# Optimization experiments

Measured on AMD Instinct MI355X. Metric: run time of the kernel, lower is better.

## Reference

```python
import jax, jax.numpy as jnp
import numpy as np

F_DIM = 256
N_HEADS = 4
D_Q = F_DIM // N_HEADS  # 64
EPS = 1e-6


def layer_norm(x, g, b):
    mu = jnp.mean(x, axis=-1, keepdims=True)
    var = jnp.mean(jnp.square(x - mu), axis=-1, keepdims=True)
    return (x - mu) * jax.lax.rsqrt(var + EPS) * g + b


def linear(x, W, b):
    # torch nn.Linear: y = x @ W.T + b, W: [out, in]
    return jnp.einsum('...i,oi->...o', x, W) + b


def setup_inputs() -> dict:
    key = jax.random.key(0)
    ks = jax.random.split(key, 16)
    f = F_DIM
    inp = {
        'code_map': jax.random.normal(ks[0], (8, 512, f), jnp.float32),
        'texture_map': jax.random.normal(ks[1], (8, 512, f), jnp.float32),
        'Wq': jax.random.normal(ks[2], (N_HEADS * D_Q, f), jnp.float32) * 0.02,
        'bq': jnp.zeros((N_HEADS * D_Q,), jnp.float32),
        'Wk': jax.random.normal(ks[3], (N_HEADS * D_Q, f), jnp.float32) * 0.02,
        'bk': jnp.zeros((N_HEADS * D_Q,), jnp.float32),
        'Wv': jax.random.normal(ks[4], (N_HEADS * D_Q, f), jnp.float32) * 0.02,
        'bv': jnp.zeros((N_HEADS * D_Q,), jnp.float32),
        'Wo': jax.random.normal(ks[5], (f, N_HEADS * D_Q), jnp.float32) * 0.02,
        'bo': jnp.zeros((f,), jnp.float32),
        'ln1_g': jnp.ones((f,), jnp.float32), 'ln1_b': jnp.zeros((f,), jnp.float32),
        'ln2_g': jnp.ones((f,), jnp.float32), 'ln2_b': jnp.zeros((f,), jnp.float32),
        'ffln_g': jnp.ones((f,), jnp.float32), 'ffln_b': jnp.zeros((f,), jnp.float32),
        'W1': jax.random.normal(ks[6], (f, f), jnp.float32) * 0.02,
        'b1': jnp.zeros((f,), jnp.float32),
        'W2': jax.random.normal(ks[7], (f, f), jnp.float32) * 0.02,
        'b2': jnp.zeros((f,), jnp.float32),
    }
    return inp


def reference(code_map, texture_map, Wq, bq, Wk, bk, Wv, bv, Wo, bo,
              ln1_g, ln1_b, ln2_g, ln2_b, ffln_g, ffln_b, W1, b1, W2, b2):
    n_code, V, f = code_map.shape
    bs = texture_map.shape[0]
    h, dq = N_HEADS, D_Q

    # LayerNorms (code side -> ln1, texture side -> ln2); expansion via repeat
    # is a pure broadcast, so keep code side [n_code,...] and texture side [bs,...].
    code2 = layer_norm(code_map, ln1_g, ln1_b)       # [n, V, f]
    tex2 = layer_norm(texture_map, ln2_g, ln2_b)     # [b, V, f]

    q = linear(tex2, Wq, bq).reshape(bs, V, h, dq)    # [b, V, h, d]
    k = linear(code2, Wk, bk).reshape(n_code, V, h, dq)
    v = linear(code2, Wv, bv).reshape(n_code, V, h, dq)

    scale = 1.0 / jnp.sqrt(jnp.asarray(dq, q.dtype))
    # scores: [b, n, h, Vq, Vk]
    scores = jnp.einsum('bqhd,nkhd->bnhqk', q, k) * scale
    attn = jax.nn.softmax(scores, axis=-1)
    ctx = jnp.einsum('bnhqk,nkhd->bnhqd', attn, v)    # [b, n, h, V, d]
    ctx = ctx.transpose(0, 1, 3, 2, 4).reshape(bs, n_code, V, h * dq)
    feat = linear(ctx, Wo, bo)                        # [b, n, V, f]

    x = texture_map[:, None, :, :] + feat             # residual with broadcast
    # ffR: MLP_res_block
    y = layer_norm(x, ffln_g, ffln_b)
    y = linear(jax.nn.relu(linear(y, W1, b1)), W2, b2)
    return x + y
```

## Files before the change

### kernel.cpp

```cpp
#include <hip/hip_runtime.h>
#include <hip/hip_bf16.h>

#define F 256
#define V 512
#define NB 8
#define NC 8
#define NH 4
#define DQ 64
#define EPS 1e-6f
#define CEXPQ 0.18033688f

typedef __hip_bfloat16 bf16;
typedef __attribute__((ext_vector_type(8))) short short8;
typedef __attribute__((ext_vector_type(4))) float f32x4;
typedef __attribute__((ext_vector_type(4))) unsigned uint4v;

__device__ __forceinline__ float b2f(bf16 x){ return __bfloat162float(x); }
__device__ __forceinline__ float shf(short s){
    return __bfloat162float(__builtin_bit_cast(bf16, (unsigned short)s));
}

#define MFMA(a,b,c) __builtin_amdgcn_mfma_f32_16x16x32_bf16((a),(b),(c),0,0,0)

__device__ __forceinline__ unsigned pack2bf(float a, float b){
    unsigned short ua = __builtin_bit_cast(unsigned short, __float2bfloat16(a));
    unsigned short ub = __builtin_bit_cast(unsigned short, __float2bfloat16(b));
    return (unsigned)ua | ((unsigned)ub << 16);
}

__global__ __launch_bounds__(256)
void qkv_kernel(const float* __restrict__ code, const float* __restrict__ tex,
                const float* __restrict__ wq_f, const float* __restrict__ wk_f,
                const float* __restrict__ wv_f, const float* __restrict__ wo_f,
                const float* __restrict__ w1_f, const float* __restrict__ w2_f,
                const float* __restrict__ ln1_g, const float* __restrict__ ln1_b,
                const float* __restrict__ ln2_g, const float* __restrict__ ln2_b,
                const float* __restrict__ bq, const float* __restrict__ bk,
                const float* __restrict__ bv,
                bf16* __restrict__ qn, bf16* __restrict__ k4, bf16* __restrict__ v4,
                bf16* __restrict__ tb, bf16* __restrict__ wbf){
    int tid = threadIdx.x;
    if (blockIdx.x >= 64){
        int flat = (blockIdx.z * 16 + (blockIdx.x - 64)) * 4 + blockIdx.y;
        int idx = flat * 1024 + tid * 4;
        int which = idx >> 16;
        const float* s = which == 0 ? wo_f : which == 1 ? w1_f : w2_f;
        int local = idx & 65535;
        float4 v = *(const float4*)(s + local);
        uint2 p; p.x = pack2bf(v.x, v.y); p.y = pack2bf(v.z, v.w);
        *(uint2*)(wbf + (3 + which) * (F * F) + local) = p;
        return;
    }

    __shared__ bf16 lnb[64][264];
    __shared__ bf16 ts[64][72];
    int which = blockIdx.z;
    const float* src  = (which == 0) ? tex : code;
    const float* g    = (which == 0) ? ln2_g : ln1_g;
    const float* be   = (which == 0) ? ln2_b : ln1_b;
    const float* wsrc = (which == 0) ? wq_f : (which == 1) ? wk_f : wv_f;
    const float* bias = (which == 0) ? bq : (which == 1) ? bk : bv;

    int w = tid >> 6, lane = tid & 63;
    int lg = lane >> 4, li = lane & 15;
    int rowbase = blockIdx.x * 64 + w * 16;
    int colbase = blockIdx.y * 64;

    float4 gg = *(const float4*)(g + lane * 4);
    float4 bb = *(const float4*)(be + lane * 4);
    bool wtb = (which == 0) && (blockIdx.y == 0);

    #pragma unroll
    for(int half = 0; half < 2; half++){
        float4 xr[8];
        #pragma unroll
        for(int r8 = 0; r8 < 8; r8++)
            xr[r8] = *(const float4*)(src + (rowbase + half * 8 + r8) * F + lane * 4);
        #pragma unroll
        for(int r8 = 0; r8 < 8; r8++){
            int row = rowbase + half * 8 + r8;
            float4 x = xr[r8];
            if (wtb){
                uint2 p; p.x = pack2bf(x.x, x.y); p.y = pack2bf(x.z, x.w);
                *(uint2*)(tb + row * F + lane * 4) = p;
            }
            float s = x.x + x.y + x.z + x.w;
            float q = x.x * x.x + x.y * x.y + x.z * x.z + x.w * x.w;
            #pragma unroll
            for(int m = 1; m < 64; m <<= 1){
                s += __shfl_xor(s, m);
                q += __shfl_xor(q, m);
            }
            float mu = s * (1.0f / F);
            float var = q * (1.0f / F) - mu * mu;
            float rs = rsqrtf(var + EPS);
            uint2 p;
            p.x = pack2bf((x.x - mu) * rs * gg.x + bb.x, (x.y - mu) * rs * gg.y + bb.y);
            p.y = pack2bf((x.z - mu) * rs * gg.z + bb.z, (x.w - mu) * rs * gg.w + bb.w);
            *(uint2*)&lnb[w * 16 + half * 8 + r8][lane * 4] = p;
        }
    }

    f32x4 acc[4];
    #pragma unroll
    for(int ni = 0; ni < 4; ni++) acc[ni] = (f32x4){0.f,0.f,0.f,0.f};

    #pragma unroll
    for(int kc = 0; kc < 8; kc++){
        short8 a = *(const short8*)&lnb[w * 16 + li][kc * 32 + lg * 8];
        #pragma unroll
        for(int ni = 0; ni < 4; ni++){
            const float* wp = wsrc + (colbase + ni * 16 + li) * F + kc * 32 + lg * 8;
            float4 b0 = *(const float4*)(wp);
            float4 b1 = *(const float4*)(wp + 4);
            uint4v ub;
            ub.x = pack2bf(b0.x, b0.y); ub.y = pack2bf(b0.z, b0.w);
            ub.z = pack2bf(b1.x, b1.y); ub.w = pack2bf(b1.z, b1.w);
            short8 bbf = __builtin_bit_cast(short8, ub);
            acc[ni] = MFMA(a, bbf, acc[ni]);
        }
    }

    float cscale = (which == 0) ? CEXPQ : 1.0f;
    if (which < 2){
        #pragma unroll
        for(int ni = 0; ni < 4; ni++)
            #pragma unroll
            for(int r = 0; r < 4; r++)
                ts[w * 16 + lg * 4 + r][ni * 16 + li] =
                    __float2bfloat16((acc[ni][r] + bias[colbase + ni * 16 + li]) * cscale);
    } else {
        #pragma unroll
        for(int ni = 0; ni < 4; ni++)
            #pragma unroll
            for(int r = 0; r < 4; r++)
                ts[ni * 16 + li][w * 16 + lg * 4 + r] =
                    __float2bfloat16(acc[ni][r] + bias[colbase + ni * 16 + li]);
    }
    __syncthreads();

    if (which == 0){
        int rr = tid >> 2, gg2 = tid & 3;
        *(short8*)(qn + (blockIdx.x * 64 + rr) * F + colbase + gg2 * 16)
            = *(const short8*)&ts[rr][gg2 * 16];
    } else if (which == 1){
        int n = blockIdx.x >> 3;
        int kc2base = (blockIdx.x & 7) * 2;
        int hh = blockIdx.y;
        #pragma unroll
        for(int rep = 0; rep < 2; rep++){
            int c = tid + 256 * rep;
            int f = c >> 6, wf = c & 63;
            int lgp = wf >> 4, lip = wf & 15;
            int kc2l = f >> 2, kt = (f >> 1) & 1, ks = f & 1;
            int keysel = ((lip >> 2) * 8) + kt * 4 + (lip & 3);
            int fi = ((n * 16 + kc2base + kc2l) * 2 + kt) * 8 + hh * 2 + ks;
            *(short8*)(k4 + fi * 512 + lgp * 128 + lip * 8)
                = *(const short8*)&ts[kc2l * 32 + keysel][ks * 32 + lgp * 8];
        }
    } else {
        int col = tid & 63, half = tid >> 6;
        int keybase = blockIdx.x * 64;
        int n = keybase >> 9;
        int keyl = (keybase & (V - 1)) + half * 16;
        int chunk = keyl >> 5, off = keyl & 31;
        *(short8*)(v4 + ((n * 16 + chunk) * F + colbase + col) * 32 + off)
            = *(const short8*)&ts[col][half * 16];
    }
}

__global__ __launch_bounds__(512) void attn_mlp_kernel(const bf16* __restrict__ qn,
                                                       const bf16* __restrict__ k4,
                                                       const bf16* __restrict__ v4,
                                                       const bf16* __restrict__ wbf,
                                                       const float* __restrict__ bo,
                                                       const bf16* __restrict__ tb,
                                                       const float* __restrict__ ffg,
                                                       const float* __restrict__ ffb,
                                                       const float* __restrict__ b1,
                                                       const float* __restrict__ b2,
                                                       float* __restrict__ out){
    __shared__ bf16 xs[64][264];
    int n = blockIdx.x & 7, b = blockIdx.x >> 3, qt = blockIdx.y;
    int tid = threadIdx.x;
    int w = tid >> 6, lane = tid & 63;
    int h = w & 3, qh = w >> 2;
    int lg = lane >> 4, li = lane & 15;

    short8 qB[2][2];
    #pragma unroll
    for(int qq = 0; qq < 2; qq++)
        #pragma unroll
        for(int ks = 0; ks < 2; ks++)
            qB[qq][ks] = *(const short8*)(qn + (b * V + qt * 64 + qh * 32 + qq * 16 + li) * F
                                             + h * DQ + ks * 32 + lg * 8);

    f32x4 o[2][4], ls[2];
    #pragma unroll
    for(int qq = 0; qq < 2; qq++){
        #pragma unroll
        for(int dt = 0; dt < 4; dt++) o[qq][dt] = (f32x4){0.f,0.f,0.f,0.f};
        ls[qq] = (f32x4){0.f,0.f,0.f,0.f};
    }

    short8 ones8;
    #pragma unroll
    for(int j = 0; j < 8; j++) ones8[j] = (short)0x3F80;

    int fel = lg * 128 + li * 8;

    #pragma unroll
    for(int kc = 0; kc < 16; kc++){
        int fb = ((n * 16 + kc) * 2) * 8 + h * 2;
        short8 kA0 = *(const short8*)(k4 + (fb + 0) * 512 + fel);
        short8 kA1 = *(const short8*)(k4 + (fb + 1) * 512 + fel);
        short8 kA2 = *(const short8*)(k4 + (fb + 8) * 512 + fel);
        short8 kA3 = *(const short8*)(k4 + (fb + 9) * 512 + fel);
        const bf16* vb = v4 + ((n * 16 + kc) * F + h * DQ) * 32;
        short8 vA0 = *(const short8*)(vb + (0 * 16 + li) * 32 + lg * 8);
        short8 vA1 = *(const short8*)(vb + (1 * 16 + li) * 32 + lg * 8);
        short8 vA2 = *(const short8*)(vb + (2 * 16 + li) * 32 + lg * 8);
        short8 vA3 = *(const short8*)(vb + (3 * 16 + li) * 32 + lg * 8);

        #pragma unroll
        for(int qq = 0; qq < 2; qq++){
            f32x4 st0 = (f32x4){0.f,0.f,0.f,0.f};
            f32x4 st1 = (f32x4){0.f,0.f,0.f,0.f};
            __builtin_amdgcn_s_setprio(1);
            st0 = MFMA(kA0, qB[qq][0], st0);
            st1 = MFMA(kA2, qB[qq][0], st1);
            st0 = MFMA(kA1, qB[qq][1], st0);
            st1 = MFMA(kA3, qB[qq][1], st1);
            __builtin_amdgcn_s_setprio(0);

            float p0[4], p1[4];
            #pragma unroll
            for(int r = 0; r < 4; r++){
                p0[r] = exp2f(st0[r]);
                p1[r] = exp2f(st1[r]);
            }

            uint4v uv;
            uv.x = pack2bf(p0[0], p0[1]);
            uv.y = pack2bf(p0[2], p0[3]);
            uv.z = pack2bf(p1[0], p1[1]);
            uv.w = pack2bf(p1[2], p1[3]);
            short8 pfrag = __builtin_bit_cast(short8, uv);

            __builtin_amdgcn_s_setprio(1);
            o[qq][0] = MFMA(vA0, pfrag, o[qq][0]);
            o[qq][1] = MFMA(vA1, pfrag, o[qq][1]);
            o[qq][2] = MFMA(vA2, pfrag, o[qq][2]);
            o[qq][3] = MFMA(vA3, pfrag, o[qq][3]);
            ls[qq] = MFMA(ones8, pfrag, ls[qq]);
            __builtin_amdgcn_s_setprio(0);
        }
    }

    float inv[2];
    #pragma unroll
    for(int qq = 0; qq < 2; qq++) inv[qq] = 1.0f / ls[qq][0];

    #pragma unroll
    for(int qq = 0; qq < 2; qq++)
        #pragma unroll
        for(int dt = 0; dt < 4; dt++){
            uint2 pkd;
            pkd.x = pack2bf(o[qq][dt][0] * inv[qq], o[qq][dt][1] * inv[qq]);
            pkd.y = pack2bf(o[qq][dt][2] * inv[qq], o[qq][dt][3] * inv[qq]);
            *(uint2*)&xs[qh * 32 + qq * 16 + li][h * DQ + dt * 16 + lg * 4] = pkd;
        }
    __syncthreads();

    const bf16* Wo = wbf + 3 * (F * F);
    int colbase = w * 32;
    f32x4 xac[4][2];
    #pragma unroll
    for(int mi = 0; mi < 4; mi++)
        #pragma unroll
        for(int ni = 0; ni < 2; ni++) xac[mi][ni] = (f32x4){0.f,0.f,0.f,0.f};
    #pragma unroll
    for(int kc = 0; kc < 8; kc++){
        short8 a[4];
        #pragma unroll
        for(int mi = 0; mi < 4; mi++)
            a[mi] = *(const short8*)&xs[mi * 16 + li][kc * 32 + lg * 8];
        #pragma unroll
        for(int ni = 0; ni < 2; ni++){
            short8 bw = *(const short8*)(Wo + (colbase + ni * 16 + li) * F + kc * 32 + lg * 8);
            #pragma unroll
            for(int mi = 0; mi < 4; mi++)
                xac[mi][ni] = MFMA(a[mi], bw, xac[mi][ni]);
        }
    }
    float xres[4][2][4];
    #pragma unroll
    for(int mi = 0; mi < 4; mi++)
        #pragma unroll
        for(int r = 0; r < 4; r++){
            int qrel = mi * 16 + lg * 4 + r;
            #pragma unroll
            for(int ni = 0; ni < 2; ni++){
                int col = colbase + ni * 16 + li;
                xres[mi][ni][r] = xac[mi][ni][r] + bo[col]
                                + b2f(tb[(b * V + qt * 64 + qrel) * F + col]);
            }
        }
    __syncthreads();
    #pragma unroll
    for(int mi = 0; mi < 4; mi++)
        #pragma unroll
        for(int r = 0; r < 4; r++){
            int qrel = mi * 16 + lg * 4 + r;
            #pragma unroll
            for(int ni = 0; ni < 2; ni++)
                xs[qrel][colbase + ni * 16 + li] = __float2bfloat16(xres[mi][ni][r]);
        }
    __syncthreads();

    int row = tid >> 3, sub = tid & 7;
    short8 xv[4];
    #pragma unroll
    for(int seg = 0; seg < 4; seg++)
        xv[seg] = *(const short8*)&xs[row][sub * 32 + seg * 8];
    float sum = 0.f, sq = 0.f;
    #pragma unroll
    for(int seg = 0; seg < 4; seg++)
        #pragma unroll
        for(int j = 0; j < 8; j++){
            float v0 = shf(xv[seg][j]);
            sum += v0; sq += v0 * v0;
        }
    #pragma unroll
    for(int m = 1; m < 8; m <<= 1){
        sum += __shfl_xor(sum, m);
        sq  += __shfl_xor(sq, m);
    }
    float mu = sum * (1.0f / F);
    float var = sq * (1.0f / F) - mu * mu;
    float rsv = rsqrtf(var + EPS);
    #pragma unroll
    for(int seg = 0; seg < 4; seg++){
        int c = sub * 32 + seg * 8;
        float4 g0 = *(const float4*)(ffg + c);
        float4 g1 = *(const float4*)(ffg + c + 4);
        float4 f0 = *(const float4*)(ffb + c);
        float4 f1 = *(const float4*)(ffb + c + 4);
        float n0 = (shf(xv[seg][0]) - mu) * rsv * g0.x + f0.x;
        float n1 = (shf(xv[seg][1]) - mu) * rsv * g0.y + f0.y;
        float n2 = (shf(xv[seg][2]) - mu) * rsv * g0.z + f0.z;
        float n3 = (shf(xv[seg][3]) - mu) * rsv * g0.w + f0.w;
        float n4 = (shf(xv[seg][4]) - mu) * rsv * g1.x + f1.x;
        float n5 = (shf(xv[seg][5]) - mu) * rsv * g1.y + f1.y;
        float n6 = (shf(xv[seg][6]) - mu) * rsv * g1.z + f1.z;
        float n7 = (shf(xv[seg][7]) - mu) * rsv * g1.w + f1.w;
        uint4v pk;
        pk.x = pack2bf(n0, n1); pk.y = pack2bf(n2, n3);
        pk.z = pack2bf(n4, n5); pk.w = pack2bf(n6, n7);
        *(short8*)&xs[row][c] = __builtin_bit_cast(short8, pk);
    }
    __syncthreads();

    const bf16* W1b = wbf + 4 * (F * F);
    f32x4 hac[4][2];
    #pragma unroll
    for(int mi = 0; mi < 4; mi++)
        #pragma unroll
        for(int ni = 0; ni < 2; ni++) hac[mi][ni] = (f32x4){0.f,0.f,0.f,0.f};
    #pragma unroll
    for(int kc = 0; kc < 8; kc++){
        short8 a[4];
        #pragma unroll
        for(int mi = 0; mi < 4; mi++)
            a[mi] = *(const short8*)&xs[mi * 16 + li][kc * 32 + lg * 8];
        #pragma unroll
        for(int ni = 0; ni < 2; ni++){
            short8 bw = *(const short8*)(W1b + (colbase + ni * 16 + li) * F + kc * 32 + lg * 8);
            #pragma unroll
            for(int mi = 0; mi < 4; mi++)
                hac[mi][ni] = MFMA(a[mi], bw, hac[mi][ni]);
        }
    }
    __syncthreads();
    #pragma unroll
    for(int mi = 0; mi < 4; mi++)
        #pragma unroll
        for(int r = 0; r < 4; r++){
            int rr = mi * 16 + lg * 4 + r;
            #pragma unroll
            for(int ni = 0; ni < 2; ni++){
                int col = colbase + ni * 16 + li;
                xs[rr][col] = __float2bfloat16(fmaxf(hac[mi][ni][r] + b1[col], 0.f));
            }
        }
    __syncthreads();

    const bf16* W2b = wbf + 5 * (F * F);
    f32x4 oac[4][2];
    #pragma unroll
    for(int mi = 0; mi < 4; mi++)
        #pragma unroll
        for(int ni = 0; ni < 2; ni++) oac[mi][ni] = (f32x4){0.f,0.f,0.f,0.f};
    #pragma unroll
    for(int kc = 0; kc < 8; kc++){
        short8 a[4];
        #pragma unroll
        for(int mi = 0; mi < 4; mi++)
            a[mi] = *(const short8*)&xs[mi * 16 + li][kc * 32 + lg * 8];
        #pragma unroll
        for(int ni = 0; ni < 2; ni++){
            short8 bw = *(const short8*)(W2b + (colbase + ni * 16 + li) * F + kc * 32 + lg * 8);
            #pragma unroll
            for(int mi = 0; mi < 4; mi++)
                oac[mi][ni] = MFMA(a[mi], bw, oac[mi][ni]);
        }
    }
    #pragma unroll
    for(int mi = 0; mi < 4; mi++)
        #pragma unroll
        for(int r = 0; r < 4; r++){
            int qrel = mi * 16 + lg * 4 + r;
            int ro = (b * NC + n) * V + qt * 64 + qrel;
            #pragma unroll
            for(int ni = 0; ni < 2; ni++){
                int col = colbase + ni * 16 + li;
                out[ro * F + col] = oac[mi][ni][r] + b2[col] + xres[mi][ni][r];
            }
        }
}

extern "C" void kernel_launch(void* const* d_in, const int* in_sizes, int n_in,
                              void* d_out, int out_size, void* d_ws, size_t ws_size,
                              hipStream_t stream) {
    const float* code_map = (const float*)d_in[0];
    const float* tex_map  = (const float*)d_in[1];
    const float* Wq = (const float*)d_in[2];  const float* bq = (const float*)d_in[3];
    const float* Wk = (const float*)d_in[4];  const float* bk = (const float*)d_in[5];
    const float* Wv = (const float*)d_in[6];  const float* bv = (const float*)d_in[7];
    const float* Wo = (const float*)d_in[8];  const float* bo = (const float*)d_in[9];
    const float* ln1_g = (const float*)d_in[10]; const float* ln1_b = (const float*)d_in[11];
    const float* ln2_g = (const float*)d_in[12]; const float* ln2_b = (const float*)d_in[13];
    const float* ffln_g = (const float*)d_in[14]; const float* ffln_b = (const float*)d_in[15];
    const float* W1 = (const float*)d_in[16]; const float* b1 = (const float*)d_in[17];
    const float* W2 = (const float*)d_in[18]; const float* b2 = (const float*)d_in[19];
    float* out = (float*)d_out;

    bf16* ws  = (bf16*)d_ws;
    bf16* qn  = ws;
    bf16* k4  = qn + 1048576;
    bf16* v4  = k4 + 1048576;
    bf16* tb  = v4 + 1048576;
    bf16* wbf = tb + 1048576;

    qkv_kernel<<<dim3(80, 4, 3), 256, 0, stream>>>(code_map, tex_map,
                                                   Wq, Wk, Wv, Wo, W1, W2,
                                                   ln1_g, ln1_b, ln2_g, ln2_b,
                                                   bq, bk, bv, qn, k4, v4, tb, wbf);
    attn_mlp_kernel<<<dim3(64, 8), 512, 0, stream>>>(qn, k4, v4, wbf, bo, tb,
                                                     ffln_g, ffln_b, b1, b2, out);
}
```

Baseline: 193.4 us.

## Halve query tile per block and split keys across wave groups

Each attention block now handles 32 query rows instead of 64. The two wave groups, which previously split the query rows, now each process half of the 512 keys. Their partial outputs and row sums are combined through a new shared-memory buffer before normalization. The grid doubles to raise block count and latency hiding, at the cost of twice as many per-block reads of the Wo/W1/W2 weights, lower MFMA reuse per weight load in the MLP stages, and extra barriers for the reduction.

New measurement: 208.8 us. 1.08x slower.

```diff
diff --git a/kernel.cpp b/kernel.cpp
--- a/kernel.cpp
+++ b/kernel.cpp
@@ -180,11 +180,12 @@
                                                        const float* __restrict__ b1,
                                                        const float* __restrict__ b2,
                                                        float* __restrict__ out){
-    __shared__ bf16 xs[64][264];
+    __shared__ bf16 xs[32][264];
+    __shared__ float rb[4][64][17];
     int n = blockIdx.x & 7, b = blockIdx.x >> 3, qt = blockIdx.y;
     int tid = threadIdx.x;
     int w = tid >> 6, lane = tid & 63;
-    int h = w & 3, qh = w >> 2;
+    int h = w & 3, c = w >> 2;
     int lg = lane >> 4, li = lane & 15;
 
     short8 qB[2][2];
@@ -192,7 +193,7 @@
     for(int qq = 0; qq < 2; qq++)
         #pragma unroll
         for(int ks = 0; ks < 2; ks++)
-            qB[qq][ks] = *(const short8*)(qn + (b * V + qt * 64 + qh * 32 + qq * 16 + li) * F
+            qB[qq][ks] = *(const short8*)(qn + (b * V + qt * 32 + qq * 16 + li) * F
                                              + h * DQ + ks * 32 + lg * 8);
 
     f32x4 o[2][4], ls[2];
@@ -210,7 +211,8 @@
     int fel = lg * 128 + li * 8;
 
     #pragma unroll
-    for(int kc = 0; kc < 16; kc++){
+    for(int i = 0; i < 8; i++){
+        int kc = c * 8 + i;
         int fb = ((n * 16 + kc) * 2) * 8 + h * 2;
         short8 kA0 = *(const short8*)(k4 + (fb + 0) * 512 + fel);
         short8 kA1 = *(const short8*)(k4 + (fb + 1) * 512 + fel);
@@ -257,45 +259,55 @@
         }
     }
 
-    float inv[2];
-    #pragma unroll
-    for(int qq = 0; qq < 2; qq++) inv[qq] = 1.0f / ls[qq][0];
-
-    #pragma unroll
-    for(int qq = 0; qq < 2; qq++)
-        #pragma unroll
-        for(int dt = 0; dt < 4; dt++){
-            uint2 pkd;
-            pkd.x = pack2bf(o[qq][dt][0] * inv[qq], o[qq][dt][1] * inv[qq]);
-            pkd.y = pack2bf(o[qq][dt][2] * inv[qq], o[qq][dt][3] * inv[qq]);
-            *(uint2*)&xs[qh * 32 + qq * 16 + li][h * DQ + dt * 16 + lg * 4] = pkd;
-        }
-    __syncthreads();
+    #pragma unroll
+    for(int qq = 0; qq < 2; qq++){
+        if (c == 1){
+            #pragma unroll
+            for(int dt = 0; dt < 4; dt++)
+                #pragma unroll
+                for(int r = 0; r < 4; r++)
+                    rb[h][lane][dt * 4 + r] = o[qq][dt][r];
+            rb[h][lane][16] = ls[qq][0];
+        }
+        __syncthreads();
+        if (c == 0){
+            float inv = 1.0f / (ls[qq][0] + rb[h][lane][16]);
+            #pragma unroll
+            for(int dt = 0; dt < 4; dt++){
+                float o0 = (o[qq][dt][0] + rb[h][lane][dt * 4 + 0]) * inv;
+                float o1 = (o[qq][dt][1] + rb[h][lane][dt * 4 + 1]) * inv;
+                float o2 = (o[qq][dt][2] + rb[h][lane][dt * 4 + 2]) * inv;
+                float o3 = (o[qq][dt][3] + rb[h][lane][dt * 4 + 3]) * inv;
+                uint2 pkd;
+                pkd.x = pack2bf(o0, o1);
+                pkd.y = pack2bf(o2, o3);
+                *(uint2*)&xs[qq * 16 + li][h * DQ + dt * 16 + lg * 4] = pkd;
+            }
+        }
+        __syncthreads();
+    }
 
     const bf16* Wo = wbf + 3 * (F * F);
     int colbase = w * 32;
-    f32x4 xac[4][2];
-    #pragma unroll
-    for(int mi = 0; mi < 4; mi++)
+    f32x4 xac[2][2];
+    #pragma unroll
+    for(int mi = 0; mi < 2; mi++)
         #pragma unroll
         for(int ni = 0; ni < 2; ni++) xac[mi][ni] = (f32x4){0.f,0.f,0.f,0.f};
     #pragma unroll
     for(int kc = 0; kc < 8; kc++){
-        short8 a[4];
-        #pragma unroll
-        for(int mi = 0; mi < 4; mi++)
-            a[mi] = *(const short8*)&xs[mi * 16 + li][kc * 32 + lg * 8];
+        short8 a0 = *(const short8*)&xs[li][kc * 32 + lg * 8];
+        short8 a1 = *(const short8*)&xs[16 + li][kc * 32 + lg * 8];
         #pragma unroll
         for(int ni = 0; ni < 2; ni++){
             short8 bw = *(const short8*)(Wo + (colbase + ni * 16 + li) * F + kc * 32 + lg * 8);
-            #pragma unroll
-            for(int mi = 0; mi < 4; mi++)
-                xac[mi][ni] = MFMA(a[mi], bw, xac[mi][ni]);
-        }
-    }
-    float xres[4][2][4];
-    #pragma unroll
-    for(int mi = 0; mi < 4; mi++)
+            xac[0][ni] = MFMA(a0, bw, xac[0][ni]);
+            xac[1][ni] = MFMA(a1, bw, xac[1][ni]);
+        }
+    }
+    float xres[2][2][4];
+    #pragma unroll
+    for(int mi = 0; mi < 2; mi++)
         #pragma unroll
         for(int r = 0; r < 4; r++){
             int qrel = mi * 16 + lg * 4 + r;
@@ -303,12 +315,12 @@
             for(int ni = 0; ni < 2; ni++){
                 int col = colbase + ni * 16 + li;
                 xres[mi][ni][r] = xac[mi][ni][r] + bo[col]
-                                + b2f(tb[(b * V + qt * 64 + qrel) * F + col]);
-            }
-        }
-    __syncthreads();
-    #pragma unroll
-    for(int mi = 0; mi < 4; mi++)
+                                + b2f(tb[(b * V + qt * 32 + qrel) * F + col]);
+            }
+        }
+    __syncthreads();
+    #pragma unroll
+    for(int mi = 0; mi < 2; mi++)
         #pragma unroll
         for(int r = 0; r < 4; r++){
             int qrel = mi * 16 + lg * 4 + r;
@@ -318,72 +330,79 @@
         }
     __syncthreads();
 
-    int row = tid >> 3, sub = tid & 7;
-    short8 xv[4];
-    #pragma unroll
-    for(int seg = 0; seg < 4; seg++)
-        xv[seg] = *(const short8*)&xs[row][sub * 32 + seg * 8];
+    int row = tid >> 4, sub = tid & 15;
+    short8 xa = *(const short8*)&xs[row][sub * 16];
+    short8 xb2 = *(const short8*)&xs[row][sub * 16 + 8];
     float sum = 0.f, sq = 0.f;
     #pragma unroll
-    for(int seg = 0; seg < 4; seg++)
-        #pragma unroll
-        for(int j = 0; j < 8; j++){
-            float v0 = shf(xv[seg][j]);
-            sum += v0; sq += v0 * v0;
-        }
-    #pragma unroll
-    for(int m = 1; m < 8; m <<= 1){
+    for(int j = 0; j < 8; j++){
+        float v0 = shf(xa[j]), v1 = shf(xb2[j]);
+        sum += v0 + v1; sq += v0 * v0 + v1 * v1;
+    }
+    #pragma unroll
+    for(int m = 1; m < 16; m <<= 1){
         sum += __shfl_xor(sum, m);
         sq  += __shfl_xor(sq, m);
     }
     float mu = sum * (1.0f / F);
     float var = sq * (1.0f / F) - mu * mu;
     float rsv = rsqrtf(var + EPS);
-    #pragma unroll
-    for(int seg = 0; seg < 4; seg++){
-        int c = sub * 32 + seg * 8;
-        float4 g0 = *(const float4*)(ffg + c);
-        float4 g1 = *(const float4*)(ffg + c + 4);
-        float4 f0 = *(const float4*)(ffb + c);
-        float4 f1 = *(const float4*)(ffb + c + 4);
-        float n0 = (shf(xv[seg][0]) - mu) * rsv * g0.x + f0.x;
-        float n1 = (shf(xv[seg][1]) - mu) * rsv * g0.y + f0.y;
-        float n2 = (shf(xv[seg][2]) - mu) * rsv * g0.z + f0.z;
-        float n3 = (shf(xv[seg][3]) - mu) * rsv * g0.w + f0.w;
-        float n4 = (shf(xv[seg][4]) - mu) * rsv * g1.x + f1.x;
-        float n5 = (shf(xv[seg][5]) - mu) * rsv * g1.y + f1.y;
-        float n6 = (shf(xv[seg][6]) - mu) * rsv * g1.z + f1.z;
-        float n7 = (shf(xv[seg][7]) - mu) * rsv * g1.w + f1.w;
-        uint4v pk;
-        pk.x = pack2bf(n0, n1); pk.y = pack2bf(n2, n3);
-        pk.z = pack2bf(n4, n5); pk.w = pack2bf(n6, n7);
-        *(short8*)&xs[row][c] = __builtin_bit_cast(short8, pk);
+    {
+        int c0 = sub * 16;
+        float4 g0 = *(const float4*)(ffg + c0);
+        float4 g1 = *(const float4*)(ffg + c0 + 4);
+        float4 g2 = *(const float4*)(ffg + c0 + 8);
+        float4 g3 = *(const float4*)(ffg + c0 + 12);
+        float4 f0 = *(const float4*)(ffb + c0);
+        float4 f1 = *(const float4*)(ffb + c0 + 4);
+        float4 f2 = *(const float4*)(ffb + c0 + 8);
+        float4 f3 = *(const float4*)(ffb + c0 + 12);
+        float n0 = (shf(xa[0]) - mu) * rsv * g0.x + f0.x;
+        float n1 = (shf(xa[1]) - mu) * rsv * g0.y + f0.y;
+        float n2 = (shf(xa[2]) - mu) * rsv * g0.z + f0.z;
+        float n3 = (shf(xa[3]) - mu) * rsv * g0.w + f0.w;
+        float n4 = (shf(xa[4]) - mu) * rsv * g1.x + f1.x;
+        float n5 = (shf(xa[5]) - mu) * rsv * g1.y + f1.y;
+        float n6 = (shf(xa[6]) - mu) * rsv * g1.z + f1.z;
+        float n7 = (shf(xa[7]) - mu) * rsv * g1.w + f1.w;
+        float m0 = (shf(xb2[0]) - mu) * rsv * g2.x + f2.x;
+        float m1 = (shf(xb2[1]) - mu) * rsv * g2.y + f2.y;
+        float m2 = (shf(xb2[2]) - mu) * rsv * g2.z + f2.z;
+        float m3 = (shf(xb2[3]) - mu) * rsv * g2.w + f2.w;
+        float m4 = (shf(xb2[4]) - mu) * rsv * g3.x + f3.x;
+        float m5 = (shf(xb2[5]) - mu) * rsv * g3.y + f3.y;
+        float m6 = (shf(xb2[6]) - mu) * rsv * g3.z + f3.z;
+        float m7 = (shf(xb2[7]) - mu) * rsv * g3.w + f3.w;
+        uint4v pa, pb;
+        pa.x = pack2bf(n0, n1); pa.y = pack2bf(n2, n3);
+        pa.z = pack2bf(n4, n5); pa.w = pack2bf(n6, n7);
+        pb.x = pack2bf(m0, m1); pb.y = pack2bf(m2, m3);
+        pb.z = pack2bf(m4, m5); pb.w = pack2bf(m6, m7);
+        *(short8*)&xs[row][sub * 16]     = __builtin_bit_cast(short8, pa);
+        *(short8*)&xs[row][sub * 16 + 8] = __builtin_bit_cast(short8, pb);
     }
     __syncthreads();
 
     const bf16* W1b = wbf + 4 * (F * F);
-    f32x4 hac[4][2];
-    #pragma unroll
-    for(int mi = 0; mi < 4; mi++)
+    f32x4 hac[2][2];
+    #pragma unroll
+    for(int mi = 0; mi < 2; mi++)
         #pragma unroll
         for(int ni = 0; ni < 2; ni++) hac[mi][ni] = (f32x4){0.f,0.f,0.f,0.f};
     #pragma unroll
     for(int kc = 0; kc < 8; kc++){
-        short8 a[4];
-        #pragma unroll
-        for(int mi = 0; mi < 4; mi++)
-            a[mi] = *(const short8*)&xs[mi * 16 + li][kc * 32 + lg * 8];
+        short8 a0 = *(const short8*)&xs[li][kc * 32 + lg * 8];
+        short8 a1 = *(const short8*)&xs[16 + li][kc * 32 + lg * 8];
         #pragma unroll
         for(int ni = 0; ni < 2; ni++){
             short8 bw = *(const short8*)(W1b + (colbase + ni * 16 + li) * F + kc * 32 + lg * 8);
-            #pragma unroll
-            for(int mi = 0; mi < 4; mi++)
-                hac[mi][ni] = MFMA(a[mi], bw, hac[mi][ni]);
-        }
-    }
-    __syncthreads();
-    #pragma unroll
-    for(int mi = 0; mi < 4; mi++)
+            hac[0][ni] = MFMA(a0, bw, hac[0][ni]);
+            hac[1][ni] = MFMA(a1, bw, hac[1][ni]);
+        }
+    }
+    __syncthreads();
+    #pragma unroll
+    for(int mi = 0; mi < 2; mi++)
         #pragma unroll
         for(int r = 0; r < 4; r++){
             int rr = mi * 16 + lg * 4 + r;
@@ -396,31 +415,28 @@
     __syncthreads();
 
     const bf16* W2b = wbf + 5 * (F * F);
-    f32x4 oac[4][2];
-    #pragma unroll
-    for(int mi = 0; mi < 4; mi++)
+    f32x4 oac[2][2];
+    #pragma unroll
+    for(int mi = 0; mi < 2; mi++)
         #pragma unroll
         for(int ni = 0; ni < 2; ni++) oac[mi][ni] = (f32x4){0.f,0.f,0.f,0.f};
     #pragma unroll
     for(int kc = 0; kc < 8; kc++){
-        short8 a[4];
-        #pragma unroll
-        for(int mi = 0; mi < 4; mi++)
-            a[mi] = *(const short8*)&xs[mi * 16 + li][kc * 32 + lg * 8];
+        short8 a0 = *(const short8*)&xs[li][kc * 32 + lg * 8];
+        short8 a1 = *(const short8*)&xs[16 + li][kc * 32 + lg * 8];
         #pragma unroll
         for(int ni = 0; ni < 2; ni++){
             short8 bw = *(const short8*)(W2b + (colbase + ni * 16 + li) * F + kc * 32 + lg * 8);
-            #pragma unroll
-            for(int mi = 0; mi < 4; mi++)
-                oac[mi][ni] = MFMA(a[mi], bw, oac[mi][ni]);
-        }
-    }
-    #pragma unroll
-    for(int mi = 0; mi < 4; mi++)
+            oac[0][ni] = MFMA(a0, bw, oac[0][ni]);
+            oac[1][ni] = MFMA(a1, bw, oac[1][ni]);
+        }
+    }
+    #pragma unroll
+    for(int mi = 0; mi < 2; mi++)
         #pragma unroll
         for(int r = 0; r < 4; r++){
             int qrel = mi * 16 + lg * 4 + r;
-            int ro = (b * NC + n) * V + qt * 64 + qrel;
+            int ro = (b * NC + n) * V + qt * 32 + qrel;
             #pragma unroll
             for(int ni = 0; ni < 2; ni++){
                 int col = colbase + ni * 16 + li;
@@ -456,6 +472,6 @@
                                                    Wq, Wk, Wv, Wo, W1, W2,
                                                    ln1_g, ln1_b, ln2_g, ln2_b,
                                                    bq, bk, bv, qn, k4, v4, tb, wbf);
-    attn_mlp_kernel<<<dim3(64, 8), 512, 0, stream>>>(qn, k4, v4, wbf, bo, tb,
-                                                     ffln_g, ffln_b, b1, b2, out);
+    attn_mlp_kernel<<<dim3(64, 16), 512, 0, stream>>>(qn, k4, v4, wbf, bo, tb,
+                                                      ffln_g, ffln_b, b1, b2, out);
 }
```
